# Performance work log

Measured on AMD Instinct MI355X. Metric: run time of the kernel, lower is better.

The kernel has to match this reference:

```python
import jax, jax.numpy as jnp
import numpy as np

HIDDEN = 1024
HEADS = 16
HEAD_DIM = HIDDEN // HEADS
B, S = 2, 2048


def setup_inputs() -> dict:
    key = jax.random.key(0)
    k1, k2, k3 = jax.random.split(key, 3)
    x = jax.random.normal(k1, (B, S, HIDDEN), dtype=jnp.float32)
    qkv_w = jax.random.normal(k2, (3 * HIDDEN, HIDDEN), dtype=jnp.float32) * (HIDDEN ** -0.5)
    out_w = jax.random.normal(k3, (HIDDEN, HIDDEN), dtype=jnp.float32) * (HIDDEN ** -0.5)
    return {"x": x, "qkv_w": qkv_w, "out_w": out_w}


def reference(x, qkv_w, out_w):
    b, s, d = x.shape
    scale = HEAD_DIM ** -0.5
    # qkv projection (Linear without bias: x @ W^T)
    qkv = x @ qkv_w.T                                   # [b, s, 3d]
    qkv = qkv.reshape(b, s, 3, HEADS, HEAD_DIM)
    qkv = jnp.transpose(qkv, (2, 0, 3, 1, 4))           # [3, b, h, s, hd]
    q, k, v = qkv[0] * scale, qkv[1], qkv[2]
    # causal attention (blocked torch loop == full causal softmax attention)
    scores = jnp.einsum('bhqd,bhkd->bhqk', q, k)        # [b, h, s, s]
    causal = jnp.tril(jnp.ones((s, s), dtype=bool))
    scores = jnp.where(causal[None, None], scores, -jnp.inf)
    weights = jax.nn.softmax(scores, axis=-1)
    attn = jnp.einsum('bhqk,bhkd->bhqd', weights, v)    # [b, h, s, hd]
    attn = jnp.transpose(attn, (0, 2, 1, 3)).reshape(b, s, d)
    return attn @ out_w.T
```

## Files before the change

### kernel.cpp

```cpp
#include <hip/hip_runtime.h>
#include <hip/hip_bf16.h>
#include <math.h>

#define HIDDEN 1024
#define HEADS 16
#define HDIM 64
#define BATCH 2
#define SEQ 2048
#define BHN (BATCH*HEADS)
#define MTOT (BATCH*SEQ)

typedef __attribute__((ext_vector_type(8))) short short8;
typedef __attribute__((ext_vector_type(4))) short short4v;
typedef __attribute__((ext_vector_type(4))) float floatx4;

#define GL2LDS(gsrc, ldst) __builtin_amdgcn_global_load_lds( \
    (const __attribute__((address_space(1))) void*)(gsrc), \
    (__attribute__((address_space(3))) void*)(ldst), 16, 0, 0)

__device__ __forceinline__ short f2bf(float f) {
  union { float f; unsigned u; } v; v.f = f;
  unsigned u = v.u;
  unsigned r = (u + 0x7fffu + ((u >> 16) & 1u)) >> 16;
  return (short)r;
}
__device__ __forceinline__ float bf2f(short s) {
  unsigned u = ((unsigned)(unsigned short)s) << 16;
  return __builtin_bit_cast(float, u);
}

__global__ __launch_bounds__(256) void cvt3_f32_bf16(
    const float* __restrict__ a, const float* __restrict__ b, const float* __restrict__ c,
    short* __restrict__ oa, short* __restrict__ ob, short* __restrict__ oc) {
  int i = blockIdx.x * 256 + threadIdx.x;
  const float* src; short* dst; int j;
  if (i < 1048576)      { src = a; dst = oa; j = i; }
  else if (i < 1835008) { src = b; dst = ob; j = i - 1048576; }
  else                  { src = c; dst = oc; j = i - 1835008; }
  float4 f = reinterpret_cast<const float4*>(src)[j];
  short4 o;
  o.x = f2bf(f.x); o.y = f2bf(f.y); o.z = f2bf(f.z); o.w = f2bf(f.w);
  reinterpret_cast<short4*>(dst)[j] = o;
}

template<int EPI, int BN>
__global__ __launch_bounds__(256) void gemm_bt(
    const short* __restrict__ A, const short* __restrict__ B,
    int M, int N, int K,
    float* __restrict__ outF,
    short* __restrict__ outQ, short* __restrict__ outK, short* __restrict__ outV)
{
  constexpr int WN = BN / 2;
  constexpr int NI = BN / 32;
  __shared__ __align__(16) short As[128*64];
  __shared__ __align__(16) short Bs[BN*64];
  const int tid = threadIdx.x;
  const int wv = tid >> 6;
  const int lane = tid & 63;
  const int l15 = lane & 15;
  const int quad = lane >> 4;
  const int swl = l15 & 7;
  const int wm = wv >> 1, wn = wv & 1;
  const int row0 = blockIdx.y * 128, col0 = blockIdx.x * BN;

  floatx4 acc[4][NI];
#pragma unroll
  for (int i = 0; i < 4; i++)
#pragma unroll
    for (int j = 0; j < NI; j++) acc[i][j] = (floatx4){0.f, 0.f, 0.f, 0.f};

  for (int k0 = 0; k0 < K; k0 += 64) {
#pragma unroll
    for (int rd = 0; rd < 4; ++rd) {
      int chunk = rd * 256 + tid;
      int r = chunk >> 3, c = ((chunk & 7) ^ (r & 7)) << 3;
      GL2LDS(A + (long)(row0 + r) * K + k0 + c, As + (rd * 256 + wv * 64) * 8);
    }
#pragma unroll
    for (int rd = 0; rd < BN / 32; ++rd) {
      int chunk = rd * 256 + tid;
      int r = chunk >> 3, c = ((chunk & 7) ^ (r & 7)) << 3;
      GL2LDS(B + (long)(col0 + r) * K + k0 + c, Bs + (rd * 256 + wv * 64) * 8);
    }
    __syncthreads();

    short8 af[4][2], bfr[NI][2];
#pragma unroll
    for (int mi = 0; mi < 4; mi++) {
      const short* ap = As + (wm * 64 + mi * 16 + l15) * 64;
#pragma unroll
      for (int kk = 0; kk < 2; kk++)
        af[mi][kk] = *(const short8*)(ap + (((kk * 4 + quad) ^ swl) << 3));
    }
#pragma unroll
    for (int ni = 0; ni < NI; ni++) {
      const short* bp = Bs + (wn * WN + ni * 16 + l15) * 64;
#pragma unroll
      for (int kk = 0; kk < 2; kk++)
        bfr[ni][kk] = *(const short8*)(bp + (((kk * 4 + quad) ^ swl) << 3));
    }
#pragma unroll
    for (int mi = 0; mi < 4; mi++)
#pragma unroll
      for (int ni = 0; ni < NI; ni++)
#pragma unroll
        for (int kk = 0; kk < 2; kk++)
          acc[mi][ni] = __builtin_amdgcn_mfma_f32_16x16x32_bf16(af[mi][kk], bfr[ni][kk], acc[mi][ni], 0, 0, 0);
    __syncthreads();
  }

  if (EPI == 2) {
#pragma unroll
    for (int mi = 0; mi < 4; mi++) {
      int rr = row0 + wm * 64 + mi * 16 + quad * 4;
#pragma unroll
      for (int ni = 0; ni < NI; ni++) {
        int cc = col0 + wn * WN + ni * 16 + l15;
#pragma unroll
        for (int r = 0; r < 4; r++)
          outF[(long)(rr + r) * N + cc] = acc[mi][ni][r];
      }
    }
  } else {
#pragma unroll
    for (int mi = 0; mi < 4; mi++) {
      int rowg = row0 + wm * 64 + mi * 16 + quad * 4;
#pragma unroll
      for (int ni = 0; ni < NI; ni++) {
        int j = col0 + wn * WN + ni * 16 + l15;
        int t = j >> 10;
        int rem = j & 1023;
        int h = rem >> 6, d = rem & 63;
#pragma unroll
        for (int r = 0; r < 4; r++) {
          int i = rowg + r;
          int b = i >> 11, s = i & 2047;
          int bh = b * HEADS + h;
          float v = acc[mi][ni][r];
          if (t == 0)      outQ[(bh * SEQ + s) * HDIM + d] = f2bf(v * 0.18033688011112042f);
          else if (t == 1) outK[(bh * SEQ + s) * HDIM + d] = f2bf(v);
          else             outV[(bh * HDIM + d) * SEQ + s] = f2bf(v);
        }
      }
    }
  }
}

__device__ __forceinline__ void stage_kv(const short* __restrict__ kg,
                                         const short* __restrict__ vT,
                                         int bh, int kt, short* KsB, short* VsB,
                                         int tid, int wv) {
#pragma unroll
  for (int i = 0; i < 4; ++i) {
    int slot = i * 128 + tid;
    int r = slot >> 3;
    int sc = ((slot & 7) ^ (r & 7)) << 3;
    GL2LDS(kg + (bh * SEQ + kt * 64 + r) * HDIM + sc, KsB + (i * 128 + wv * 64) * 8);
    GL2LDS(vT + (bh * HDIM + r) * SEQ + kt * 64 + sc, VsB + (i * 128 + wv * 64) * 8);
  }
}

__global__ __launch_bounds__(128, 2) void flash_attn(
    const short* __restrict__ qg, const short* __restrict__ kg,
    const short* __restrict__ vT, short* __restrict__ attn,
    short* __restrict__ partO, float* __restrict__ partL)
{
  __shared__ __align__(16) short Ks[2][64 * 64];
  __shared__ __align__(16) short Vs[2][64 * 64];

  const int tid = threadIdx.x;
  const int wv = tid >> 6, lane = tid & 63;
  const int l15 = lane & 15, quad = lane >> 4;
  const int swl = l15 & 7;

  const int g = blockIdx.x;
  const int band = g / 96, j = g % 96;
  int bh, rt, kt0, kt1, half = 0;
  bool psplit;
  if (j < 64) {
    rt = 31 - band; bh = j >> 1; half = j & 1;
    const int n = rt + 1, n0 = (n + 1) >> 1;
    kt0 = half ? n0 : 0; kt1 = half ? n : n0;
    psplit = true;
  } else {
    rt = 15 - band; bh = j - 64;
    kt0 = 0; kt1 = rt + 1;
    psplit = false;
  }
  const int m0 = rt * 64 + wv * 32;

  short8 aq[2][2];
#pragma unroll
  for (int mi = 0; mi < 2; mi++) {
    const short* qp = qg + (long)(bh * SEQ + m0 + mi * 16 + l15) * HDIM + quad * 8;
    aq[mi][0] = *(const short8*)qp;
    aq[mi][1] = *(const short8*)(qp + 32);
  }

  const short ONE = (short)0x3F80;
  const short4v ones4 = {ONE, ONE, ONE, ONE};

  floatx4 o[2][4], lsum[2];
#pragma unroll
  for (int mi = 0; mi < 2; mi++) {
    lsum[mi] = (floatx4){0.f, 0.f, 0.f, 0.f};
#pragma unroll
    for (int nt = 0; nt < 4; nt++) o[mi][nt] = (floatx4){0.f, 0.f, 0.f, 0.f};
  }

  const int nk = kt1 - kt0;
  stage_kv(kg, vT, bh, kt0, Ks[0], Vs[0], tid, wv);

  for (int i = 0; i < nk; ++i) {
    const int kt = kt0 + i;
    __syncthreads();
    const int buf = i & 1;
    if (i + 1 < nk)
      stage_kv(kg, vT, bh, kt + 1, Ks[buf ^ 1], Vs[buf ^ 1], tid, wv);

    const short* KsB = Ks[buf];
    const short* VsB = Vs[buf];

    floatx4 sc[2][4];
#pragma unroll
    for (int mi = 0; mi < 2; mi++)
#pragma unroll
      for (int nh = 0; nh < 4; nh++) sc[mi][nh] = (floatx4){0.f, 0.f, 0.f, 0.f};
#pragma unroll
    for (int nh = 0; nh < 4; nh++) {
      const short* kp = KsB + (nh * 16 + l15) * 64;
      short8 kf0 = *(const short8*)(kp + ((quad ^ swl) << 3));
      short8 kf1 = *(const short8*)(kp + (((4 + quad) ^ swl) << 3));
#pragma unroll
      for (int mi = 0; mi < 2; mi++) {
        sc[mi][nh] = __builtin_amdgcn_mfma_f32_16x16x32_bf16(kf0, aq[mi][0], sc[mi][nh], 0, 0, 0);
        sc[mi][nh] = __builtin_amdgcn_mfma_f32_16x16x32_bf16(kf1, aq[mi][1], sc[mi][nh], 0, 0, 0);
      }
    }

    short4v pa[2][4];
#pragma unroll
    for (int mi = 0; mi < 2; mi++) {
      const int qrow = m0 + mi * 16 + l15;
      const bool full = (kt * 64 + 63) <= (m0 + mi * 16);
#pragma unroll
      for (int nh = 0; nh < 4; nh++) {
        unsigned u[4];
#pragma unroll
        for (int r = 0; r < 4; r++) {
          float pe = __builtin_amdgcn_exp2f(sc[mi][nh][r]);
          if (!full) {
            const int kpos = kt * 64 + nh * 16 + quad * 4 + r;
            pe = (kpos <= qrow) ? pe : 0.f;
          }
          u[r] = __builtin_bit_cast(unsigned, pe) & 0xffff0000u;
        }
        uint2 w;
        w.x = (u[0] >> 16) | u[1];
        w.y = (u[2] >> 16) | u[3];
        pa[mi][nh] = __builtin_bit_cast(short4v, w);
      }
    }

#pragma unroll
    for (int kk = 0; kk < 4; kk++) {
      short4v bv[4];
#pragma unroll
      for (int nt = 0; nt < 4; nt++) {
        const int ch = (kk * 2 + (quad >> 1)) ^ swl;
        bv[nt] = *(const short4v*)(VsB + (nt * 16 + l15) * 64 + (ch << 3) + ((quad & 1) << 2));
      }
#pragma unroll
      for (int mi = 0; mi < 2; mi++) {
        lsum[mi] = __builtin_amdgcn_mfma_f32_16x16x16bf16_1k(pa[mi][kk], ones4, lsum[mi], 0, 0, 0);
#pragma unroll
        for (int nt = 0; nt < 4; nt++)
          o[mi][nt] = __builtin_amdgcn_mfma_f32_16x16x16bf16_1k(pa[mi][kk], bv[nt], o[mi][nt], 0, 0, 0);
      }
    }
  }

  if (!psplit) {
    const int b = bh >> 4, h = bh & 15;
#pragma unroll
    for (int mi = 0; mi < 2; mi++)
#pragma unroll
      for (int r = 0; r < 4; r++) {
        const float inv = 1.0f / lsum[mi][r];
        const int s = m0 + mi * 16 + quad * 4 + r;
#pragma unroll
        for (int nt = 0; nt < 4; nt++)
          attn[(long)(b * SEQ + s) * HIDDEN + h * HDIM + nt * 16 + l15] = f2bf(o[mi][nt][r] * inv);
      }
  } else {
    const int set = (bh * 16 + (rt - 16)) * 2 + half;
    short* po = partO + (long)set * 4096;
    float* pl = partL + set * 64;
#pragma unroll
    for (int mi = 0; mi < 2; mi++)
#pragma unroll
      for (int r = 0; r < 4; r++) {
        const int qloc = wv * 32 + mi * 16 + quad * 4 + r;
#pragma unroll
        for (int nt = 0; nt < 4; nt++)
          po[qloc * 64 + nt * 16 + l15] = f2bf(o[mi][nt][r]);
        if (l15 == 0) pl[qloc] = lsum[mi][r];
      }
  }
}

__global__ __launch_bounds__(256) void combine(
    const short* __restrict__ partO, const float* __restrict__ partL,
    short* __restrict__ attn)
{
  const int g = blockIdx.x;
  const int bh = g & 31, r16 = g >> 5;
  const int rt = 16 + r16;
  const int setA = (bh * 16 + r16) * 2;
  const int row = threadIdx.x >> 2, seg = (threadIdx.x & 3) << 4;
  const short* pa = partO + (long)setA * 4096 + row * 64 + seg;
  const short* pb = pa + 4096;
  const float inv = 1.0f / (partL[setA * 64 + row] + partL[(setA + 1) * 64 + row]);
  const int b = bh >> 4, h = bh & 15;
  const int s = rt * 64 + row;
  short* dst = attn + (long)(b * SEQ + s) * HIDDEN + h * HDIM + seg;
  short8 va0 = *(const short8*)pa, vb0 = *(const short8*)pb;
  short8 va1 = *(const short8*)(pa + 8), vb1 = *(const short8*)(pb + 8);
  short8 o0, o1;
#pragma unroll
  for (int i = 0; i < 8; i++) {
    o0[i] = f2bf((bf2f(va0[i]) + bf2f(vb0[i])) * inv);
    o1[i] = f2bf((bf2f(va1[i]) + bf2f(vb1[i])) * inv);
  }
  *(short8*)dst = o0;
  *(short8*)(dst + 8) = o1;
}

extern "C" void kernel_launch(void* const* d_in, const int* in_sizes, int n_in,
                              void* d_out, int out_size, void* d_ws, size_t ws_size,
                              hipStream_t stream) {
  const float* x     = (const float*)d_in[0];
  const float* qkv_w = (const float*)d_in[1];
  const float* out_w = (const float*)d_in[2];
  float* out = (float*)d_out;

  short* xb    = (short*)d_ws;
  short* wqb   = xb  + MTOT * HIDDEN;
  short* wob   = wqb + 3 * HIDDEN * HIDDEN;
  short* qB    = wob + HIDDEN * HIDDEN;
  short* kB    = qB  + BHN * SEQ * HDIM;
  short* vTB   = kB  + BHN * SEQ * HDIM;
  short* attn  = vTB + BHN * SEQ * HDIM;
  short* partO = attn + MTOT * HIDDEN;
  float* partL = (float*)(partO + 1024 * 4096);

  cvt3_f32_bf16<<<dim3(8192), dim3(256), 0, stream>>>(x, qkv_w, out_w, xb, wqb, wob);

  gemm_bt<1, 128><<<dim3(3 * HIDDEN / 128, MTOT / 128), dim3(256), 0, stream>>>(
      xb, wqb, MTOT, 3 * HIDDEN, HIDDEN, nullptr, qB, kB, vTB);

  flash_attn<<<dim3(1536), dim3(128), 0, stream>>>(qB, kB, vTB, attn, partO, partL);
  combine<<<dim3(512), dim3(256), 0, stream>>>(partO, partL, attn);

  gemm_bt<2, 64><<<dim3(HIDDEN / 64, MTOT / 128), dim3(256), 0, stream>>>(
      attn, wob, MTOT, HIDDEN, HIDDEN, out, nullptr, nullptr, nullptr);
}
```

Before: 183.8 us.

## Drop LDS staging in flash attention; load K/V directly to registers

Removes the shared-memory double buffer and __syncthreads from the attention loop. K fragments are now loaded from global memory straight into registers with a software prefetch of the next tile, and V fragments are read directly per tile. The PV product switches from 16x16x16 to 16x16x32 MFMA by concatenating P fragments. The block-to-work mapping is also changed so blocks are interleaved across heads. This trades LDS traffic and barriers for more global/L2 loads and higher register pressure, with V loads no longer prefetched ahead of use.

```diff
diff --git a/kernel.cpp b/kernel.cpp
--- a/kernel.cpp
+++ b/kernel.cpp
@@ -27,6 +27,9 @@
 __device__ __forceinline__ float bf2f(short s) {
   unsigned u = ((unsigned)(unsigned short)s) << 16;
   return __builtin_bit_cast(float, u);
+}
+__device__ __forceinline__ short8 cat4(short4v a, short4v b) {
+  return __builtin_shufflevector(a, b, 0, 1, 2, 3, 4, 5, 6, 7);
 }
 
 __global__ __launch_bounds__(256) void cvt3_f32_bf16(
@@ -146,48 +149,34 @@
   }
 }
 
-__device__ __forceinline__ void stage_kv(const short* __restrict__ kg,
-                                         const short* __restrict__ vT,
-                                         int bh, int kt, short* KsB, short* VsB,
-                                         int tid, int wv) {
-#pragma unroll
-  for (int i = 0; i < 4; ++i) {
-    int slot = i * 128 + tid;
-    int r = slot >> 3;
-    int sc = ((slot & 7) ^ (r & 7)) << 3;
-    GL2LDS(kg + (bh * SEQ + kt * 64 + r) * HDIM + sc, KsB + (i * 128 + wv * 64) * 8);
-    GL2LDS(vT + (bh * HDIM + r) * SEQ + kt * 64 + sc, VsB + (i * 128 + wv * 64) * 8);
-  }
-}
-
 __global__ __launch_bounds__(128, 2) void flash_attn(
     const short* __restrict__ qg, const short* __restrict__ kg,
     const short* __restrict__ vT, short* __restrict__ attn,
     short* __restrict__ partO, float* __restrict__ partL)
 {
-  __shared__ __align__(16) short Ks[2][64 * 64];
-  __shared__ __align__(16) short Vs[2][64 * 64];
-
   const int tid = threadIdx.x;
   const int wv = tid >> 6, lane = tid & 63;
   const int l15 = lane & 15, quad = lane >> 4;
-  const int swl = l15 & 7;
 
   const int g = blockIdx.x;
-  const int band = g / 96, j = g % 96;
-  int bh, rt, kt0, kt1, half = 0;
+  const int cls = g & 7, r = g >> 3;
+  const int bh = cls + 8 * (r & 3);
+  const int it = r >> 2;
+  int rt, kt0, kt1, kh = 0;
   bool psplit;
-  if (j < 64) {
-    rt = 31 - band; bh = j >> 1; half = j & 1;
+  if (it < 32) {
+    rt = 31 - (it >> 1); kh = it & 1;
     const int n = rt + 1, n0 = (n + 1) >> 1;
-    kt0 = half ? n0 : 0; kt1 = half ? n : n0;
+    kt0 = kh ? n0 : 0; kt1 = kh ? n : n0;
     psplit = true;
   } else {
-    rt = 15 - band; bh = j - 64;
-    kt0 = 0; kt1 = rt + 1;
+    rt = 47 - it; kt0 = 0; kt1 = rt + 1;
     psplit = false;
   }
   const int m0 = rt * 64 + wv * 32;
+
+  const short* kbase = kg + (long)bh * SEQ * HDIM;
+  const short* vbase = vT + (long)bh * HDIM * SEQ;
 
   short8 aq[2][2];
 #pragma unroll
@@ -198,7 +187,7 @@
   }
 
   const short ONE = (short)0x3F80;
-  const short4v ones4 = {ONE, ONE, ONE, ONE};
+  const short8 ones8 = {ONE, ONE, ONE, ONE, ONE, ONE, ONE, ONE};
 
   floatx4 o[2][4], lsum[2];
 #pragma unroll
@@ -209,17 +198,28 @@
   }
 
   const int nk = kt1 - kt0;
-  stage_kv(kg, vT, bh, kt0, Ks[0], Vs[0], tid, wv);
-
-  for (int i = 0; i < nk; ++i) {
-    const int kt = kt0 + i;
-    __syncthreads();
-    const int buf = i & 1;
-    if (i + 1 < nk)
-      stage_kv(kg, vT, bh, kt + 1, Ks[buf ^ 1], Vs[buf ^ 1], tid, wv);
-
-    const short* KsB = Ks[buf];
-    const short* VsB = Vs[buf];
+  short8 kf[2][4][2];
+#pragma unroll
+  for (int nh = 0; nh < 4; nh++) {
+    const short* kp = kbase + (kt0 * 64 + nh * 16 + l15) * HDIM + quad * 8;
+    kf[0][nh][0] = *(const short8*)kp;
+    kf[0][nh][1] = *(const short8*)(kp + 32);
+  }
+
+  for (int i2 = 0; i2 < nk; ++i2) {
+    const int kt = kt0 + i2;
+    const int cur = i2 & 1;
+
+    short4v vlo[4][2], vhi[4][2];
+#pragma unroll
+    for (int nt = 0; nt < 4; nt++) {
+      const short* vp = vbase + (nt * 16 + l15) * SEQ + kt * 64 + quad * 4;
+#pragma unroll
+      for (int g32 = 0; g32 < 2; g32++) {
+        vlo[nt][g32] = *(const short4v*)(vp + g32 * 32);
+        vhi[nt][g32] = *(const short4v*)(vp + g32 * 32 + 16);
+      }
+    }
 
     floatx4 sc[2][4];
 #pragma unroll
@@ -227,14 +227,19 @@
 #pragma unroll
       for (int nh = 0; nh < 4; nh++) sc[mi][nh] = (floatx4){0.f, 0.f, 0.f, 0.f};
 #pragma unroll
-    for (int nh = 0; nh < 4; nh++) {
-      const short* kp = KsB + (nh * 16 + l15) * 64;
-      short8 kf0 = *(const short8*)(kp + ((quad ^ swl) << 3));
-      short8 kf1 = *(const short8*)(kp + (((4 + quad) ^ swl) << 3));
+    for (int nh = 0; nh < 4; nh++)
 #pragma unroll
       for (int mi = 0; mi < 2; mi++) {
-        sc[mi][nh] = __builtin_amdgcn_mfma_f32_16x16x32_bf16(kf0, aq[mi][0], sc[mi][nh], 0, 0, 0);
-        sc[mi][nh] = __builtin_amdgcn_mfma_f32_16x16x32_bf16(kf1, aq[mi][1], sc[mi][nh], 0, 0, 0);
+        sc[mi][nh] = __builtin_amdgcn_mfma_f32_16x16x32_bf16(kf[cur][nh][0], aq[mi][0], sc[mi][nh], 0, 0, 0);
+        sc[mi][nh] = __builtin_amdgcn_mfma_f32_16x16x32_bf16(kf[cur][nh][1], aq[mi][1], sc[mi][nh], 0, 0, 0);
+      }
+
+    if (i2 + 1 < nk) {
+#pragma unroll
+      for (int nh = 0; nh < 4; nh++) {
+        const short* kp = kbase + ((kt + 1) * 64 + nh * 16 + l15) * HDIM + quad * 8;
+        kf[cur ^ 1][nh][0] = *(const short8*)kp;
+        kf[cur ^ 1][nh][1] = *(const short8*)(kp + 32);
       }
     }
 
@@ -247,13 +252,13 @@
       for (int nh = 0; nh < 4; nh++) {
         unsigned u[4];
 #pragma unroll
-        for (int r = 0; r < 4; r++) {
-          float pe = __builtin_amdgcn_exp2f(sc[mi][nh][r]);
+        for (int r2 = 0; r2 < 4; r2++) {
+          float pe = __builtin_amdgcn_exp2f(sc[mi][nh][r2]);
           if (!full) {
-            const int kpos = kt * 64 + nh * 16 + quad * 4 + r;
+            const int kpos = kt * 64 + nh * 16 + quad * 4 + r2;
             pe = (kpos <= qrow) ? pe : 0.f;
           }
-          u[r] = __builtin_bit_cast(unsigned, pe) & 0xffff0000u;
+          u[r2] = __builtin_bit_cast(unsigned, pe) & 0xffff0000u;
         }
         uint2 w;
         w.x = (u[0] >> 16) | u[1];
@@ -263,19 +268,15 @@
     }
 
 #pragma unroll
-    for (int kk = 0; kk < 4; kk++) {
-      short4v bv[4];
-#pragma unroll
-      for (int nt = 0; nt < 4; nt++) {
-        const int ch = (kk * 2 + (quad >> 1)) ^ swl;
-        bv[nt] = *(const short4v*)(VsB + (nt * 16 + l15) * 64 + (ch << 3) + ((quad & 1) << 2));
-      }
+    for (int g32 = 0; g32 < 2; g32++) {
 #pragma unroll
       for (int mi = 0; mi < 2; mi++) {
-        lsum[mi] = __builtin_amdgcn_mfma_f32_16x16x16bf16_1k(pa[mi][kk], ones4, lsum[mi], 0, 0, 0);
+        const short8 a32 = cat4(pa[mi][2 * g32], pa[mi][2 * g32 + 1]);
+        lsum[mi] = __builtin_amdgcn_mfma_f32_16x16x32_bf16(a32, ones8, lsum[mi], 0, 0, 0);
 #pragma unroll
         for (int nt = 0; nt < 4; nt++)
-          o[mi][nt] = __builtin_amdgcn_mfma_f32_16x16x16bf16_1k(pa[mi][kk], bv[nt], o[mi][nt], 0, 0, 0);
+          o[mi][nt] = __builtin_amdgcn_mfma_f32_16x16x32_bf16(
+              a32, cat4(vlo[nt][g32], vhi[nt][g32]), o[mi][nt], 0, 0, 0);
       }
     }
   }
@@ -285,26 +286,26 @@
 #pragma unroll
     for (int mi = 0; mi < 2; mi++)
 #pragma unroll
-      for (int r = 0; r < 4; r++) {
-        const float inv = 1.0f / lsum[mi][r];
-        const int s = m0 + mi * 16 + quad * 4 + r;
+      for (int r2 = 0; r2 < 4; r2++) {
+        const float inv = 1.0f / lsum[mi][r2];
+        const int s = m0 + mi * 16 + quad * 4 + r2;
 #pragma unroll
         for (int nt = 0; nt < 4; nt++)
-          attn[(long)(b * SEQ + s) * HIDDEN + h * HDIM + nt * 16 + l15] = f2bf(o[mi][nt][r] * inv);
+          attn[(long)(b * SEQ + s) * HIDDEN + h * HDIM + nt * 16 + l15] = f2bf(o[mi][nt][r2] * inv);
       }
   } else {
-    const int set = (bh * 16 + (rt - 16)) * 2 + half;
+    const int set = (bh * 16 + (rt - 16)) * 2 + kh;
     short* po = partO + (long)set * 4096;
     float* pl = partL + set * 64;
 #pragma unroll
     for (int mi = 0; mi < 2; mi++)
 #pragma unroll
-      for (int r = 0; r < 4; r++) {
-        const int qloc = wv * 32 + mi * 16 + quad * 4 + r;
+      for (int r2 = 0; r2 < 4; r2++) {
+        const int qloc = wv * 32 + mi * 16 + quad * 4 + r2;
 #pragma unroll
         for (int nt = 0; nt < 4; nt++)
-          po[qloc * 64 + nt * 16 + l15] = f2bf(o[mi][nt][r]);
-        if (l15 == 0) pl[qloc] = lsum[mi][r];
+          po[qloc * 64 + nt * 16 + l15] = f2bf(o[mi][nt][r2]);
+        if (l15 == 0) pl[qloc] = lsum[mi][r2];
       }
   }
 }
```

New measurement: 304.9 us. 65.9% more time.
